# Kernel optimization log

Hardware: AMD Instinct MI355X
Metric: run time of the kernel (lower is better)

The kernel has to match this reference:

```python
import jax, jax.numpy as jnp
import numpy as np

N = 2000      # num_of_vertices
T = 12        # history
B = 4         # batch
C = 32        # in_dim == out_dims[i]
STRIDES = 3
L = 3         # len(out_dims)
W_WIN = T - STRIDES + 1  # 10 sliding windows


def setup_inputs() -> dict:
    key = jax.random.key(0)
    ks = jax.random.split(key, 12)
    adj_scale = 2.0 / (3 * N)  # keep row sums ~1 so activations stay in range
    fc_scale = 1.0 / np.sqrt(C)
    g_scale = 1.0 / np.sqrt(2 * C)
    return {
        "x": jax.random.normal(ks[0], (B, T, N, C), jnp.float32),
        "adj": jax.random.uniform(ks[1], (3 * N, 3 * N), jnp.float32) * adj_scale,
        "temporal_adj": jax.random.uniform(ks[2], (N, N), jnp.float32) * adj_scale,
        "temporal_embedding": jax.random.normal(ks[3], (1, T, 1, C), jnp.float32) * 0.0003,
        "spatial_embedding": jax.random.normal(ks[4], (1, 1, N, C), jnp.float32) * 0.0003,
        "W_fc": jax.random.normal(ks[5], (W_WIN, L, C, 2 * C), jnp.float32) * fc_scale,
        "b_fc": jnp.zeros((W_WIN, L, 2 * C), jnp.float32),
        "Wr": jax.random.normal(ks[6], (2 * C, C), jnp.float32) * g_scale,
        "br": jnp.zeros((C,), jnp.float32),
        "Wu": jax.random.normal(ks[7], (2 * C, C), jnp.float32) * g_scale,
        "bu": jnp.zeros((C,), jnp.float32),
        "Wn": jax.random.normal(ks[8], (2 * C, C), jnp.float32) * g_scale,
        "bn": jnp.zeros((C,), jnp.float32),
        "Wo": jax.random.normal(ks[9], (C, C), jnp.float32) * (1.0 / np.sqrt(C)),
        "bo": jnp.zeros((C,), jnp.float32),
    }


def _forward(x, adj, temporal_adj, temporal_embedding, spatial_embedding,
             W_fc, b_fc, Wr, br, Wu, bu, Wn, bn, Wo, bo):
    # x: (B, T, N, C)
    x = x + temporal_embedding + spatial_embedding

    # Patch the 3Nx3N adjacency: 4 corner N x N blocks become temporal_adj
    A = adj.at[:N, :N].set(temporal_adj)
    A = A.at[2 * N:, 2 * N:].set(temporal_adj)
    A = A.at[2 * N:, :N].set(temporal_adj)
    A = A.at[:N, 2 * N:].set(temporal_adj)

    # Extract all sliding windows at once: (B, W, 3, N, C)
    idx = jnp.arange(W_WIN)[:, None] + jnp.arange(STRIDES)[None, :]
    xw = x[:, idx]
    # -> (W, 3N, B, C) matching torch reshape(B, 3*N, C).permute(1,0,2)
    h = jnp.transpose(xw, (1, 2, 3, 0, 4)).reshape(W_WIN, STRIDES * N, B, C)

    # STSGCM stack (per-window weights), GLU activation
    layer_mid = []
    for l in range(L):
        h = jnp.einsum('nm,wmbc->wnbc', A, h)                 # graph conv
        z = jnp.einsum('wnbc,wcd->wnbd', h, W_fc[:, l]) + b_fc[:, l][:, None, None, :]
        lhs, rhs = jnp.split(z, 2, axis=-1)
        h = lhs * jax.nn.sigmoid(rhs)                         # GLU
        layer_mid.append(h[:, N:2 * N])                       # middle time slice (W, N, B, C)
    out = jnp.max(jnp.stack(layer_mid, axis=0), axis=0)      # max over layers
    out = jnp.transpose(out, (2, 0, 1, 3))                    # (B, W, N, C)

    # GRU-style gating across the W time slices (note: next hidden is yt)
    def step(hid, inp):
        comb = jnp.concatenate([inp, hid], axis=-1)
        reset = jax.nn.sigmoid(comb @ Wr + br)
        update = jax.nn.sigmoid(comb @ Wu + bu)
        comb_new = jnp.concatenate([inp, reset * hid], axis=-1)
        new_mem = jnp.tanh(comb_new @ Wn + bn)
        output = update * hid + (1.0 - update) * new_mem
        yt = jax.nn.sigmoid(output @ Wo + bo)
        return yt, output

    h0 = jnp.zeros((B, N, C), x.dtype)
    _, residual = jax.lax.scan(step, h0, jnp.transpose(out, (1, 0, 2, 3)))
    residual = jnp.transpose(residual, (1, 0, 2, 3))          # (B, W, N, C)
    return out + residual


def reference(x, adj, temporal_adj, temporal_embedding, spatial_embedding,
              W_fc, b_fc, Wr, br, Wu, bu, Wn, bn, Wo, bo):
    return _forward(x, adj, temporal_adj, temporal_embedding, spatial_embedding,
                    W_fc, b_fc, Wr, br, Wu, bu, Wn, bn, Wo, bo)
```

## Files before the change

### kernel.cpp

```cpp
#include <hip/hip_runtime.h>
#include <hip/hip_bf16.h>

#define N_NODE 2000
#define BB 4
#define CC 32
#define LL 3
#define WW 10
#define M3 6000
#define MP 6016
#define KP 6016
#define NCOL 1280

typedef __bf16 bf16x8 __attribute__((ext_vector_type(8)));
typedef float f32x4 __attribute__((ext_vector_type(4)));

__device__ __forceinline__ float sigmoidf_(float x) { return 1.0f / (1.0f + __expf(-x)); }
__device__ __forceinline__ float tanhf_(float x) { return 1.0f - 2.0f / (__expf(2.0f * x) + 1.0f); }

__global__ __launch_bounds__(256) void k_build_A(const float* __restrict__ adj,
                                                 const float* __restrict__ tadj,
                                                 __hip_bfloat16* __restrict__ A) {
  const int m = blockIdx.x * 256 + threadIdx.x;
  const int n = blockIdx.y;
  if (m >= KP) return;
  float v = 0.0f;
  if (n < M3 && m < M3) {
    const bool nr = (n < N_NODE) | (n >= 2 * N_NODE);
    const bool mr = (m < N_NODE) | (m >= 2 * N_NODE);
    if (nr & mr) {
      const int nn = (n >= 2 * N_NODE) ? n - 2 * N_NODE : n;
      const int mm = (m >= 2 * N_NODE) ? m - 2 * N_NODE : m;
      v = tadj[(size_t)nn * N_NODE + mm];
    } else {
      v = adj[(size_t)n * M3 + m];
    }
  }
  A[(size_t)n * KP + m] = __float2bfloat16(v);
}

__global__ __launch_bounds__(256) void k_build_H(const float* __restrict__ x,
                                                 const float* __restrict__ temb,
                                                 const float* __restrict__ semb,
                                                 __hip_bfloat16* __restrict__ H) {
  const int m = blockIdx.x * 256 + threadIdx.x;
  const int col = blockIdx.y;
  if (m >= KP) return;
  float v = 0.0f;
  if (m < M3) {
    const int w = col >> 7, b = (col >> 5) & 3, c = col & 31;
    const int s = (m >= 2 * N_NODE) ? 2 : (m >= N_NODE ? 1 : 0);
    const int n = m - s * N_NODE;
    const int tt = w + s;
    v = x[(((size_t)b * 12 + tt) * N_NODE + n) * CC + c] + temb[tt * CC + c] +
        semb[(size_t)n * CC + c];
  }
  H[(size_t)col * KP + m] = __float2bfloat16(v);
}

__global__ __launch_bounds__(256) void k_gemm(const __hip_bfloat16* __restrict__ A,
                                              const __hip_bfloat16* __restrict__ Bt,
                                              float* __restrict__ G) {
  __shared__ __align__(16) __hip_bfloat16 lA[128][72];
  __shared__ __align__(16) __hip_bfloat16 lB[128][72];
  const int tid = threadIdx.x;
  const int lane = tid & 63;
  const int wv = tid >> 6;
  const int wr = wv >> 1, wc = wv & 1;
  const long row0 = (long)blockIdx.x * 128;
  const long col0 = (long)blockIdx.y * 128;

  const int srow = tid >> 3;
  const int scol = tid & 7;
  const char* gA = (const char*)A;
  const char* gB = (const char*)Bt;

  const int rrow = lane & 15;
  const int koff = (lane >> 4) << 4;

  f32x4 acc[4][4] = {};

  const int NKT = KP / 64;
  for (int kt = 0; kt < NKT; ++kt) {
    __syncthreads();
#pragma unroll
    for (int i = 0; i < 4; ++i) {
      const int r = i * 32 + srow;
      const size_t goff = (size_t)kt * 128 + (size_t)scol * 16;
      bf16x8 va = *(const bf16x8*)(gA + (size_t)(row0 + r) * (KP * 2) + goff);
      bf16x8 vb = *(const bf16x8*)(gB + (size_t)(col0 + r) * (KP * 2) + goff);
      *(bf16x8*)((char*)&lA[r][0] + scol * 16) = va;
      *(bf16x8*)((char*)&lB[r][0] + scol * 16) = vb;
    }
    __syncthreads();
#pragma unroll
    for (int ks = 0; ks < 2; ++ks) {
      bf16x8 af[4], bfr[4];
#pragma unroll
      for (int mi = 0; mi < 4; ++mi)
        af[mi] = *(const bf16x8*)((const char*)&lA[wr * 64 + mi * 16 + rrow][0] + ks * 64 + koff);
#pragma unroll
      for (int ni = 0; ni < 4; ++ni)
        bfr[ni] = *(const bf16x8*)((const char*)&lB[wc * 64 + ni * 16 + rrow][0] + ks * 64 + koff);
#pragma unroll
      for (int mi = 0; mi < 4; ++mi)
#pragma unroll
        for (int ni = 0; ni < 4; ++ni)
          acc[mi][ni] =
              __builtin_amdgcn_mfma_f32_16x16x32_bf16(af[mi], bfr[ni], acc[mi][ni], 0, 0, 0);
    }
  }
  const int crow = (lane >> 4) * 4;
  const int ccol = lane & 15;
#pragma unroll
  for (int mi = 0; mi < 4; ++mi) {
#pragma unroll
    for (int ni = 0; ni < 4; ++ni) {
      const long r = row0 + wr * 64 + mi * 16 + crow;
      const long cix = col0 + wc * 64 + ni * 16 + ccol;
      float* gp = G + (size_t)r * NCOL + cix;
#pragma unroll
      for (int j = 0; j < 4; ++j) gp[(size_t)j * NCOL] = acc[mi][ni][j];
    }
  }
}

__global__ __launch_bounds__(256) void k_fcglu(const float* __restrict__ G,
                                               const float* __restrict__ Wfc,
                                               const float* __restrict__ bfc,
                                               __hip_bfloat16* __restrict__ Hn,
                                               float* __restrict__ outb, int l, int writeH) {
  __shared__ float sW[32 * 64];
  __shared__ float sb[64];
  const int w = blockIdx.y;
  const int t = threadIdx.x;
  const float* Ws = Wfc + (size_t)(w * LL + l) * 32 * 64;
#pragma unroll
  for (int i = 0; i < 8; ++i) sW[t + 256 * i] = Ws[t + 256 * i];
  if (t < 64) sb[t] = bfc[(size_t)(w * LL + l) * 64 + t];
  __syncthreads();
  const int nl = t >> 2, b = t & 3;
  const int n = blockIdx.x * 64 + nl;
  const int colbase = w * 128 + b * 32;
  if (n >= M3) {
    if (writeH) {
      for (int c = 0; c < 32; ++c) Hn[(size_t)(colbase + c) * KP + n] = __float2bfloat16(0.0f);
    }
    return;
  }
  const float* g = G + (size_t)n * NCOL + colbase;
  float z[64];
#pragma unroll
  for (int d = 0; d < 64; ++d) z[d] = sb[d];
  for (int c = 0; c < 32; ++c) {
    const float gv = g[c];
#pragma unroll
    for (int d = 0; d < 64; ++d) z[d] = fmaf(gv, sW[c * 64 + d], z[d]);
  }
  float h[32];
#pragma unroll
  for (int c = 0; c < 32; ++c) h[c] = z[c] * sigmoidf_(z[32 + c]);
  if (writeH) {
#pragma unroll
    for (int c = 0; c < 32; ++c) Hn[(size_t)(colbase + c) * KP + n] = __float2bfloat16(h[c]);
  }
  if (n >= N_NODE && n < 2 * N_NODE) {
    float* op = outb + (((size_t)b * WW + w) * N_NODE + (n - N_NODE)) * CC;
    if (l == 0) {
#pragma unroll
      for (int c = 0; c < 32; ++c) op[c] = h[c];
    } else {
#pragma unroll
      for (int c = 0; c < 32; ++c) op[c] = fmaxf(op[c], h[c]);
    }
  }
}

__global__ __launch_bounds__(256) void k_gru(float* __restrict__ outb, float* __restrict__ state,
                                             const float* __restrict__ Wr,
                                             const float* __restrict__ brr,
                                             const float* __restrict__ Wu,
                                             const float* __restrict__ bu,
                                             const float* __restrict__ Wn,
                                             const float* __restrict__ bnn,
                                             const float* __restrict__ Wo,
                                             const float* __restrict__ bo, int w) {
  __shared__ float sI[8][32], sH[8][32], sT[8][32];
  const int t = threadIdx.x;
  const int g = t >> 5, c = t & 31;
  const int n = blockIdx.x * 8 + g;
  const int b = blockIdx.y;
  const size_t oix = (((size_t)b * WW + w) * N_NODE + n) * CC + c;
  const size_t hix = ((size_t)b * N_NODE + n) * CC + c;
  const float inp = outb[oix];
  const float hid = state[hix];
  sI[g][c] = inp;
  sH[g][c] = hid;
  __syncthreads();
  float ar = brr[c], au = bu[c];
#pragma unroll 4
  for (int d = 0; d < 32; ++d) {
    const float i_ = sI[g][d], h_ = sH[g][d];
    ar = fmaf(i_, Wr[d * 32 + c], ar);
    ar = fmaf(h_, Wr[(32 + d) * 32 + c], ar);
    au = fmaf(i_, Wu[d * 32 + c], au);
    au = fmaf(h_, Wu[(32 + d) * 32 + c], au);
  }
  const float r = sigmoidf_(ar), u = sigmoidf_(au);
  sT[g][c] = r * hid;
  __syncthreads();
  float an = bnn[c];
#pragma unroll 4
  for (int d = 0; d < 32; ++d) {
    an = fmaf(sI[g][d], Wn[d * 32 + c], an);
    an = fmaf(sT[g][d], Wn[(32 + d) * 32 + c], an);
  }
  const float nm = tanhf_(an);
  const float outv = u * hid + (1.0f - u) * nm;
  __syncthreads();
  sT[g][c] = outv;
  __syncthreads();
  float ay = bo[c];
#pragma unroll 4
  for (int d = 0; d < 32; ++d) ay = fmaf(sT[g][d], Wo[d * 32 + c], ay);
  state[hix] = sigmoidf_(ay);
  outb[oix] = inp + outv;
}

extern "C" void kernel_launch(void* const* d_in, const int* in_sizes, int n_in, void* d_out,
                              int out_size, void* d_ws, size_t ws_size, hipStream_t stream) {
  const float* x = (const float*)d_in[0];
  const float* adj = (const float*)d_in[1];
  const float* tadj = (const float*)d_in[2];
  const float* temb = (const float*)d_in[3];
  const float* semb = (const float*)d_in[4];
  const float* Wfc = (const float*)d_in[5];
  const float* bfc = (const float*)d_in[6];
  const float* Wr = (const float*)d_in[7];
  const float* brr = (const float*)d_in[8];
  const float* Wu = (const float*)d_in[9];
  const float* bu = (const float*)d_in[10];
  const float* Wn = (const float*)d_in[11];
  const float* bnn = (const float*)d_in[12];
  const float* Wo = (const float*)d_in[13];
  const float* bo = (const float*)d_in[14];
  float* outb = (float*)d_out;

  char* ws = (char*)d_ws;
  const size_t szA = (size_t)MP * KP * 2;
  const size_t szH = (size_t)NCOL * KP * 2;
  const size_t szG = (size_t)MP * NCOL * 4;
  const size_t szS = (size_t)BB * N_NODE * CC * 4;
  if (ws_size < szA + 2 * szH + szG + szS) return;

  __hip_bfloat16* A = (__hip_bfloat16*)ws;
  __hip_bfloat16* H0 = (__hip_bfloat16*)(ws + szA);
  __hip_bfloat16* H1 = (__hip_bfloat16*)(ws + szA + szH);
  float* G = (float*)(ws + szA + 2 * szH);
  float* state = (float*)(ws + szA + 2 * szH + szG);

  hipMemsetAsync(state, 0, szS, stream);
  k_build_A<<<dim3(24, KP), 256, 0, stream>>>(adj, tadj, A);
  k_build_H<<<dim3(24, NCOL), 256, 0, stream>>>(x, temb, semb, H0);

  __hip_bfloat16* Hc = H0;
  __hip_bfloat16* Hx = H1;
  for (int l = 0; l < LL; ++l) {
    k_gemm<<<dim3(47, 10), 256, 0, stream>>>(A, Hc, G);
    k_fcglu<<<dim3(94, 10), 256, 0, stream>>>(G, Wfc, bfc, Hx, outb, l, l < 2 ? 1 : 0);
    __hip_bfloat16* tmp = Hc;
    Hc = Hx;
    Hx = tmp;
  }
  for (int w = 0; w < WW; ++w)
    k_gru<<<dim3(250, BB), 256, 0, stream>>>(outb, state, Wr, brr, Wu, bu, Wn, bnn, Wo, bo, w);
}
```

Baseline: 907.1 us.

## Use direct global-to-LDS loads with XOR swizzle and XCD block remap in GEMM

The GEMM now stages A and B tiles with global_load_lds (direct global-to-LDS DMA) instead of going through registers. It replaces the padded LDS layout with an XOR-swizzled 128-byte row layout to avoid bank conflicts, and remaps block IDs so neighbouring tiles land on the same XCD for better L2 reuse. The adjacency build kernel is also vectorised to handle 8 elements per thread. The swizzle must stay consistent between the DMA writes and the fragment reads, and the 8-wide adj loads assume alignment and no crossing of the corner-block boundary.

```diff
diff --git a/kernel.cpp b/kernel.cpp
--- a/kernel.cpp
+++ b/kernel.cpp
@@ -13,6 +13,7 @@
 
 typedef __bf16 bf16x8 __attribute__((ext_vector_type(8)));
 typedef float f32x4 __attribute__((ext_vector_type(4)));
+typedef unsigned short ushort8 __attribute__((ext_vector_type(8)));
 
 __device__ __forceinline__ float sigmoidf_(float x) { return 1.0f / (1.0f + __expf(-x)); }
 __device__ __forceinline__ float tanhf_(float x) { return 1.0f - 2.0f / (__expf(2.0f * x) + 1.0f); }
@@ -20,22 +21,30 @@
 __global__ __launch_bounds__(256) void k_build_A(const float* __restrict__ adj,
                                                  const float* __restrict__ tadj,
                                                  __hip_bfloat16* __restrict__ A) {
-  const int m = blockIdx.x * 256 + threadIdx.x;
+  const int m8 = blockIdx.x * 256 + threadIdx.x;
+  const int m = m8 * 8;
   const int n = blockIdx.y;
   if (m >= KP) return;
-  float v = 0.0f;
+  ushort8 out = {0, 0, 0, 0, 0, 0, 0, 0};
   if (n < M3 && m < M3) {
     const bool nr = (n < N_NODE) | (n >= 2 * N_NODE);
     const bool mr = (m < N_NODE) | (m >= 2 * N_NODE);
+    const float* src;
     if (nr & mr) {
       const int nn = (n >= 2 * N_NODE) ? n - 2 * N_NODE : n;
       const int mm = (m >= 2 * N_NODE) ? m - 2 * N_NODE : m;
-      v = tadj[(size_t)nn * N_NODE + mm];
+      src = tadj + (size_t)nn * N_NODE + mm;
     } else {
-      v = adj[(size_t)n * M3 + m];
-    }
-  }
-  A[(size_t)n * KP + m] = __float2bfloat16(v);
+      src = adj + (size_t)n * M3 + m;
+    }
+#pragma unroll
+    for (int j = 0; j < 8; ++j) {
+      union { __hip_bfloat16 h; unsigned short u; } cv;
+      cv.h = __float2bfloat16(src[j]);
+      out[j] = cv.u;
+    }
+  }
+  *(ushort8*)(A + (size_t)n * KP + m) = out;
 }
 
 __global__ __launch_bounds__(256) void k_build_H(const float* __restrict__ x,
@@ -60,47 +69,62 @@
 __global__ __launch_bounds__(256) void k_gemm(const __hip_bfloat16* __restrict__ A,
                                               const __hip_bfloat16* __restrict__ Bt,
                                               float* __restrict__ G) {
-  __shared__ __align__(16) __hip_bfloat16 lA[128][72];
-  __shared__ __align__(16) __hip_bfloat16 lB[128][72];
+  __shared__ __align__(16) char lA[128 * 128];
+  __shared__ __align__(16) char lB[128 * 128];
   const int tid = threadIdx.x;
   const int lane = tid & 63;
   const int wv = tid >> 6;
   const int wr = wv >> 1, wc = wv & 1;
-  const long row0 = (long)blockIdx.x * 128;
-  const long col0 = (long)blockIdx.y * 128;
-
-  const int srow = tid >> 3;
-  const int scol = tid & 7;
-  const char* gA = (const char*)A;
-  const char* gB = (const char*)Bt;
+
+  const int bid = blockIdx.x + 47 * blockIdx.y;
+  const int q = 470 / 8, r = 470 % 8;
+  const int xcd = bid & 7, lid = bid >> 3;
+  const int swz = (xcd < r ? xcd * (q + 1) : r * (q + 1) + (xcd - r) * q) + lid;
+  const int bx = swz % 47;
+  const int by = swz / 47;
+  const long row0 = (long)bx * 128;
+  const long col0 = (long)by * 128;
+
+  const int srow = wv * 32 + (lane >> 3);
+  const int soff = ((lane & 7) ^ (lane >> 3)) << 4;
+  const char* gA = (const char*)A + (size_t)(row0 + srow) * (KP * 2) + soff;
+  const char* gB = (const char*)Bt + (size_t)(col0 + srow) * (KP * 2) + soff;
+  const size_t rstep = (size_t)8 * KP * 2;
 
   const int rrow = lane & 15;
-  const int koff = (lane >> 4) << 4;
+  const int off0 = (((lane >> 4) << 4)) ^ ((lane & 7) << 4);
+  const int off1 = (64 | ((lane >> 4) << 4)) ^ ((lane & 7) << 4);
 
   f32x4 acc[4][4] = {};
 
   const int NKT = KP / 64;
   for (int kt = 0; kt < NKT; ++kt) {
     __syncthreads();
+    const char* ga = gA + (size_t)kt * 128;
+    const char* gb = gB + (size_t)kt * 128;
 #pragma unroll
     for (int i = 0; i < 4; ++i) {
-      const int r = i * 32 + srow;
-      const size_t goff = (size_t)kt * 128 + (size_t)scol * 16;
-      bf16x8 va = *(const bf16x8*)(gA + (size_t)(row0 + r) * (KP * 2) + goff);
-      bf16x8 vb = *(const bf16x8*)(gB + (size_t)(col0 + r) * (KP * 2) + goff);
-      *(bf16x8*)((char*)&lA[r][0] + scol * 16) = va;
-      *(bf16x8*)((char*)&lB[r][0] + scol * 16) = vb;
+      __builtin_amdgcn_global_load_lds(
+          (const __attribute__((address_space(1))) void*)(ga + (size_t)i * rstep),
+          (__attribute__((address_space(3))) void*)(lA + wv * 4096 + i * 1024), 16, 0, 0);
+    }
+#pragma unroll
+    for (int i = 0; i < 4; ++i) {
+      __builtin_amdgcn_global_load_lds(
+          (const __attribute__((address_space(1))) void*)(gb + (size_t)i * rstep),
+          (__attribute__((address_space(3))) void*)(lB + wv * 4096 + i * 1024), 16, 0, 0);
     }
     __syncthreads();
 #pragma unroll
     for (int ks = 0; ks < 2; ++ks) {
+      const int offk = ks ? off1 : off0;
       bf16x8 af[4], bfr[4];
 #pragma unroll
       for (int mi = 0; mi < 4; ++mi)
-        af[mi] = *(const bf16x8*)((const char*)&lA[wr * 64 + mi * 16 + rrow][0] + ks * 64 + koff);
+        af[mi] = *(const bf16x8*)(lA + (wr * 64 + mi * 16 + rrow) * 128 + offk);
 #pragma unroll
       for (int ni = 0; ni < 4; ++ni)
-        bfr[ni] = *(const bf16x8*)((const char*)&lB[wc * 64 + ni * 16 + rrow][0] + ks * 64 + koff);
+        bfr[ni] = *(const bf16x8*)(lB + (wc * 64 + ni * 16 + rrow) * 128 + offk);
 #pragma unroll
       for (int mi = 0; mi < 4; ++mi)
 #pragma unroll
@@ -115,9 +139,9 @@
   for (int mi = 0; mi < 4; ++mi) {
 #pragma unroll
     for (int ni = 0; ni < 4; ++ni) {
-      const long r = row0 + wr * 64 + mi * 16 + crow;
+      const long r_ = row0 + wr * 64 + mi * 16 + crow;
       const long cix = col0 + wc * 64 + ni * 16 + ccol;
-      float* gp = G + (size_t)r * NCOL + cix;
+      float* gp = G + (size_t)r_ * NCOL + cix;
 #pragma unroll
       for (int j = 0; j < 4; ++j) gp[(size_t)j * NCOL] = acc[mi][ni][j];
     }
@@ -259,7 +283,7 @@
   float* state = (float*)(ws + szA + 2 * szH + szG);
 
   hipMemsetAsync(state, 0, szS, stream);
-  k_build_A<<<dim3(24, KP), 256, 0, stream>>>(adj, tadj, A);
+  k_build_A<<<dim3(3, KP), 256, 0, stream>>>(adj, tadj, A);
   k_build_H<<<dim3(24, NCOL), 256, 0, stream>>>(x, temb, semb, H0);
 
   __hip_bfloat16* Hc = H0;
```

After: 882.2 us. -2.8%, faster.
